# Optimization experiments

Measured on AMD Instinct MI355X. Metric: run time of the kernel, lower is better.

The kernel has to match this reference:

```python
import jax, jax.numpy as jnp
import numpy as np

EPS = 1e-5

def _lin(x, w, b):
    return x @ w + b

def _ln(x, scale, bias):
    m = jnp.mean(x, axis=-1, keepdims=True)
    v = jnp.var(x, axis=-1, keepdims=True)
    return (x - m) / jnp.sqrt(v + EPS) * scale + bias

def setup_inputs() -> dict:
    key = jax.random.key(0)
    B, N, F, OUT, TRI = 4, 128, 128, 128, 8
    ks = iter(jax.random.split(key, 64))
    def lin_params(fan_in, fan_out):
        s = 1.0 / np.sqrt(fan_in)
        w = jax.random.uniform(next(ks), (fan_in, fan_out), minval=-s, maxval=s, dtype=jnp.float32)
        b = jax.random.uniform(next(ks), (fan_out,), minval=-s, maxval=s, dtype=jnp.float32)
        return w, b
    inp = {}
    inp['node_fts'] = jax.random.normal(next(ks), (B, N, F), dtype=jnp.float32)
    inp['edge_fts'] = jax.random.normal(next(ks), (B, N, N, F), dtype=jnp.float32)
    inp['graph_fts'] = jax.random.normal(next(ks), (B, F), dtype=jnp.float32)
    inp['hidden'] = jax.random.normal(next(ks), (B, N, F), dtype=jnp.float32)
    inp['adj_matrix'] = jax.random.randint(next(ks), (B, N, N), 0, 2, dtype=jnp.int32)
    inp['m1_w'], inp['m1_b'] = lin_params(2 * F, OUT)
    inp['m2_w'], inp['m2_b'] = lin_params(2 * F, OUT)
    inp['me_w'], inp['me_b'] = lin_params(F, OUT)
    inp['mg_w'], inp['mg_b'] = lin_params(F, OUT)
    inp['mlp1_w'], inp['mlp1_b'] = lin_params(OUT, OUT)
    inp['mlp2_w'], inp['mlp2_b'] = lin_params(OUT, OUT)
    inp['o1_w'], inp['o1_b'] = lin_params(2 * F, OUT)
    inp['o2_w'], inp['o2_b'] = lin_params(OUT, OUT)
    inp['t1_w'], inp['t1_b'] = lin_params(2 * F, TRI)
    inp['t2_w'], inp['t2_b'] = lin_params(2 * F, TRI)
    inp['te1_w'], inp['te1_b'] = lin_params(F, TRI)
    inp['te2_w'], inp['te2_b'] = lin_params(F, TRI)
    inp['te3_w'], inp['te3_b'] = lin_params(F, TRI)
    inp['tg_w'], inp['tg_b'] = lin_params(F, TRI)
    inp['o3_w'], inp['o3_b'] = lin_params(TRI, OUT)
    inp['norm_scale'] = jnp.ones((OUT,), dtype=jnp.float32)
    inp['norm_bias'] = jnp.zeros((OUT,), dtype=jnp.float32)
    return inp

def reference(node_fts, edge_fts, graph_fts, hidden, adj_matrix,
              m1_w, m1_b, m2_w, m2_b, me_w, me_b, mg_w, mg_b,
              mlp1_w, mlp1_b, mlp2_w, mlp2_b,
              o1_w, o1_b, o2_w, o2_b,
              t1_w, t1_b, t2_w, t2_b,
              te1_w, te1_b, te2_w, te2_b, te3_w, te3_b,
              tg_w, tg_b, o3_w, o3_b, norm_scale, norm_bias):
    z = jnp.concatenate([node_fts, hidden], axis=-1)          # [B,N,2F]
    msg_1 = _lin(z, m1_w, m1_b)                                # [B,N,H]
    msg_2 = _lin(z, m2_w, m2_b)
    msg_e = _lin(edge_fts, me_w, me_b)                         # [B,N,N,H]
    msg_g = _lin(graph_fts, mg_w, mg_b)                        # [B,H]
    msgs = msg_1[:, None, :, :] + msg_2[:, :, None, :] + msg_e + msg_g[:, None, None, :]
    # msg_mlp: ReLU -> Linear -> ReLU -> Linear
    msgs = _lin(jax.nn.relu(_lin(jax.nn.relu(msgs), mlp1_w, mlp1_b)), mlp2_w, mlp2_b)
    # triplet messages (note: original code reuses t_1 for tri_3 -- faithful)
    tri_1 = _lin(z, t1_w, t1_b)                                # [B,N,T]
    tri_2 = _lin(z, t2_w, t2_b)
    tri_3 = _lin(z, t1_w, t1_b)
    tri_e_1 = _lin(edge_fts, te1_w, te1_b)                     # [B,N,N,T]
    tri_e_2 = _lin(edge_fts, te2_w, te2_b)
    tri_e_3 = _lin(edge_fts, te3_w, te3_b)
    tri_g = _lin(graph_fts, tg_w, tg_b)                        # [B,T]
    triplets = (tri_1[:, :, None, None, :] + tri_2[:, None, :, None, :]
                + tri_3[:, None, None, :, :]
                + tri_e_1[:, :, :, None, :] + tri_e_2[:, :, None, :, :]
                + tri_e_3[:, None, :, :, :]
                + tri_g[:, None, None, None, :])               # [B,N,N,N,T]
    tri_msgs = _lin(jnp.max(triplets, axis=1), o3_w, o3_b)     # [B,N,N,OUT]
    tri_msgs = _ln(jax.nn.relu(tri_msgs), norm_scale, norm_bias)
    # masked max aggregation
    maxarg = jnp.where(adj_matrix[..., None] == 1, msgs, -1e9)
    msgs_agg = jnp.max(maxarg, axis=1)                         # [B,N,H]
    out = jax.nn.relu(_lin(z, o1_w, o1_b) + _lin(msgs_agg, o2_w, o2_b))
    out = _ln(out, norm_scale, norm_bias)
    return out, tri_msgs
```

## Files before the change

kernel.cpp:

```cpp
#include <hip/hip_runtime.h>
#include <hip/hip_bf16.h>
#include <cstddef>
#include <cstdint>
#include <cstring>

typedef __attribute__((ext_vector_type(8))) short bf16x8;
typedef __attribute__((ext_vector_type(4))) float f32x4;
typedef unsigned short ushort_t;

__device__ __forceinline__ ushort_t f2b(float f) {
    uint32_t x = __float_as_uint(f);
    uint32_t r = (x + 0x7FFFu + ((x >> 16) & 1u)) >> 16;
    return (ushort_t)r;
}
__device__ __forceinline__ float b2f(ushort_t u) {
    return __uint_as_float(((uint32_t)u) << 16);
}
__device__ __forceinline__ uint32_t pk2(float x, float y) {
    __hip_bfloat162 h = __float22bfloat162_rn(float2{x, y});
    uint32_t u;
    __builtin_memcpy(&u, &h, 4);
    return u;
}

__global__ void prep_kernel(const float* __restrict__ m1_w, const float* __restrict__ m2_w,
                            const float* __restrict__ o1_w, const float* __restrict__ t1_w,
                            const float* __restrict__ t2_w,
                            const float* __restrict__ me_w, const float* __restrict__ mlp1_w,
                            const float* __restrict__ mlp2_w,
                            const float* __restrict__ te1_w, const float* __restrict__ te2_w,
                            const float* __restrict__ te3_w,
                            const float* __restrict__ graph_fts,
                            const float* __restrict__ mg_w, const float* __restrict__ mg_b,
                            const float* __restrict__ m1_b,
                            const float* __restrict__ tg_w, const float* __restrict__ t2_b,
                            const float* __restrict__ tg_b,
                            ushort_t* __restrict__ Wnt,
                            ushort_t* __restrict__ Wme, ushort_t* __restrict__ Wm1,
                            ushort_t* __restrict__ Wm2, ushort_t* __restrict__ TEt,
                            float* __restrict__ G1, float* __restrict__ TG) {
    int idx = blockIdx.x * 256 + threadIdx.x;
    if (idx < 106496) {
        int o = idx >> 8, k = idx & 255;
        float v = 0.0f;
        if (o < 128)       v = m1_w[k * 128 + o];
        else if (o < 256)  v = m2_w[k * 128 + (o - 128)];
        else if (o < 384)  v = o1_w[k * 128 + (o - 256)];
        else if (o < 392)  v = t1_w[k * 8 + (o - 384)];
        else if (o < 400)  v = t2_w[k * 8 + (o - 392)];
        Wnt[idx] = f2b(v);
    } else if (idx < 122880) {
        int t = idx - 106496, o = t >> 7, h = t & 127;
        Wme[t] = f2b(me_w[h * 128 + o]);
    } else if (idx < 139264) {
        int t = idx - 122880, o = t >> 7, h = t & 127;
        Wm1[t] = f2b(mlp1_w[h * 128 + o]);
    } else if (idx < 155648) {
        int t = idx - 139264, o = t >> 7, h = t & 127;
        Wm2[t] = f2b(mlp2_w[h * 128 + o]);
    } else if (idx < 159744) {
        int t = idx - 155648, c = t >> 7, h = t & 127;
        float v = 0.0f;
        if (c < 8)       v = te1_w[h * 8 + c];
        else if (c < 16) v = te2_w[h * 8 + (c - 8)];
        else if (c < 24) v = te3_w[h * 8 + (c - 16)];
        TEt[t] = f2b(v);
    } else if (idx < 160256) {
        int t = idx - 159744, b = t >> 7, h = t & 127;
        float a = m1_b[h] + mg_b[h];
        #pragma unroll 4
        for (int k = 0; k < 128; k++) a = fmaf(graph_fts[b * 128 + k], mg_w[k * 128 + h], a);
        G1[t] = a;
    } else if (idx < 160288) {
        int t = idx - 160256, b = t >> 3, tt = t & 7;
        float a = t2_b[tt] + tg_b[tt];
        #pragma unroll 4
        for (int k = 0; k < 128; k++) a = fmaf(graph_fts[b * 128 + k], tg_w[k * 8 + tt], a);
        TG[t] = a;
    }
}

__global__ __launch_bounds__(256)
void node_gemm(const float* __restrict__ node_fts, const float* __restrict__ hidden,
               const ushort_t* __restrict__ Wnt,
               const float* __restrict__ G1, const float* __restrict__ m2_b,
               const float* __restrict__ o1_b, const float* __restrict__ t1_b,
               const float* __restrict__ TG,
               float* __restrict__ M1, float* __restrict__ M2, float* __restrict__ O1z,
               float* __restrict__ T1v, float* __restrict__ TT2) {
    __shared__ ushort_t Zs[32 * 256];
    char* Zb = (char*)Zs;
    const int tid = threadIdx.x;
    const int blk = blockIdx.x;
    const int rowblk = blk >> 1, colh = blk & 1;
    const int b = rowblk >> 2, q = rowblk & 3;
    const int row0 = b * 128 + q * 32;
    const int w = tid >> 6, l = tid & 63, g = l >> 4, lq = l & 15;

    const float4* nsrc = reinterpret_cast<const float4*>(node_fts + (size_t)row0 * 128);
    const float4* hsrc = reinterpret_cast<const float4*>(hidden + (size_t)row0 * 128);
    #pragma unroll
    for (int p = 0; p < 8; p++) {
        int idx = tid + p * 256;
        int r = idx >> 6, c4 = idx & 63;
        float4 v = (c4 < 32) ? nsrc[r * 32 + c4] : hsrc[r * 32 + (c4 - 32)];
        uint2 pk;
        pk.x = pk2(v.x, v.y);
        pk.y = pk2(v.z, v.w);
        *reinterpret_cast<uint2*>(Zb + r * 512 + (((c4 >> 1) ^ (r & 7)) << 4) + (c4 & 1) * 8) = pk;
    }
    __syncthreads();

    for (int mt = colh * 13 + w; mt < colh * 13 + 13; mt += 4) {
        f32x4 acc0 = (f32x4){0.f, 0.f, 0.f, 0.f};
        f32x4 acc1 = (f32x4){0.f, 0.f, 0.f, 0.f};
        const ushort_t* arow = Wnt + (size_t)(mt * 16 + lq) * 256;
        #pragma unroll
        for (int ks = 0; ks < 8; ks++) {
            bf16x8 a = *reinterpret_cast<const bf16x8*>(arow + ks * 32 + g * 8);
            int j0 = lq, j1 = 16 + lq;
            bf16x8 b0 = *reinterpret_cast<const bf16x8*>(Zb + j0 * 512 + (((ks * 4 + g) ^ (j0 & 7)) << 4));
            bf16x8 b1 = *reinterpret_cast<const bf16x8*>(Zb + j1 * 512 + (((ks * 4 + g) ^ (j1 & 7)) << 4));
            acc0 = __builtin_amdgcn_mfma_f32_16x16x32_bf16(a, b0, acc0, 0, 0, 0);
            acc1 = __builtin_amdgcn_mfma_f32_16x16x32_bf16(a, b1, acc1, 0, 0, 0);
        }
        #pragma unroll
        for (int half = 0; half < 2; half++) {
            const f32x4 acc = half ? acc1 : acc0;
            const int grow = row0 + half * 16 + lq;
            #pragma unroll
            for (int c = 0; c < 4; c++) {
                int o = mt * 16 + g * 4 + c;
                float v = acc[c];
                if (o < 128)       M1[(size_t)grow * 128 + o] = v + G1[b * 128 + o];
                else if (o < 256)  M2[(size_t)grow * 128 + (o - 128)] = v + m2_b[o - 128];
                else if (o < 384)  O1z[(size_t)grow * 128 + (o - 256)] = v + o1_b[o - 256];
                else if (o < 392)  T1v[(size_t)grow * 8 + (o - 384)] = v + t1_b[o - 384];
                else if (o < 400)  TT2[(size_t)grow * 8 + (o - 392)] = v + TG[b * 8 + (o - 392)];
            }
        }
    }
}

__device__ __forceinline__ void mmv(const ushort_t* __restrict__ Wt, const char* Xa,
                                    f32x4 acc[2][4], int o_blk, int j_blk, int g, int lq) {
    #pragma unroll
    for (int ks = 0; ks < 4; ks++) {
        bf16x8 a[2], bb[4];
        #pragma unroll
        for (int m = 0; m < 2; m++)
            a[m] = *reinterpret_cast<const bf16x8*>(Wt + (size_t)(o_blk + m * 16 + lq) * 128 + ks * 32 + g * 8);
        #pragma unroll
        for (int n = 0; n < 4; n++) {
            int j = j_blk + n * 16 + lq;
            bb[n] = *reinterpret_cast<const bf16x8*>(Xa + j * 256 + (((ks * 4 + g) ^ (j & 7)) << 4));
        }
        #pragma unroll
        for (int m = 0; m < 2; m++)
            #pragma unroll
            for (int n = 0; n < 4; n++)
                acc[m][n] = __builtin_amdgcn_mfma_f32_16x16x32_bf16(a[m], bb[n], acc[m][n], 0, 0, 0);
    }
}

__global__ __launch_bounds__(512, 4)
void edge_kernel(const float* __restrict__ edge_fts,
                 const ushort_t* __restrict__ Wme, const float* __restrict__ me_b,
                 const ushort_t* __restrict__ Wm1, const float* __restrict__ mlp1_b,
                 const ushort_t* __restrict__ Wm2, const float* __restrict__ mlp2_b,
                 const ushort_t* __restrict__ TEt,
                 const float* __restrict__ te1_b, const float* __restrict__ te2_b,
                 const float* __restrict__ te3_b,
                 const float* __restrict__ M1,  const float* __restrict__ M2,
                 const float* __restrict__ T1v, const float* __restrict__ TT2,
                 const int* __restrict__ adj, const float* __restrict__ O1z,
                 const float* __restrict__ o2_w, const float* __restrict__ o2_b,
                 const float* __restrict__ nsc, const float* __restrict__ nbi,
                 float* __restrict__ out,
                 ushort_t* __restrict__ T1buf, ushort_t* __restrict__ T2buf,
                 ushort_t* __restrict__ E3buf) {
    __shared__ ushort_t Xs[2][16384];
    char* X0 = (char*)Xs[0];
    char* X1 = (char*)Xs[1];
    const int tid = threadIdx.x;
    const int b  = blockIdx.x >> 7;
    const int jf = blockIdx.x & 127;
    const int w = tid >> 6, l = tid & 63, g = l >> 4, lq = l & 15;
    const int o_blk = (w & 3) * 32, j_blk = (w >> 2) * 64;

    #pragma unroll
    for (int p = 0; p < 8; p++) {
        int idx = tid + p * 512;
        int r = idx >> 5, c4 = idx & 31;
        const float4* src = reinterpret_cast<const float4*>(
            edge_fts + ((size_t)(b * 128 + r) * 128 + jf) * 128);
        float4 v = src[c4];
        uint2 pk;
        pk.x = pk2(v.x, v.y);
        pk.y = pk2(v.z, v.w);
        *reinterpret_cast<uint2*>(X0 + r * 256 + (((c4 >> 1) ^ (r & 7)) << 4) + (c4 & 1) * 8) = pk;
    }
    __syncthreads();

    {
        const int m_te = w & 1;
        const int jq = (w >> 1) & 3;
        const ushort_t* At = TEt + m_te * 16 * 128;
        f32x4 acc2[2];
        #pragma unroll
        for (int n = 0; n < 2; n++) acc2[n] = (f32x4){0.f, 0.f, 0.f, 0.f};
        #pragma unroll
        for (int ks = 0; ks < 4; ks++) {
            bf16x8 a = *reinterpret_cast<const bf16x8*>(At + lq * 128 + ks * 32 + g * 8);
            #pragma unroll
            for (int n = 0; n < 2; n++) {
                int j = jq * 32 + n * 16 + lq;
                bf16x8 bbv = *reinterpret_cast<const bf16x8*>(X0 + j * 256 + (((ks * 4 + g) ^ (j & 7)) << 4));
                acc2[n] = __builtin_amdgcn_mfma_f32_16x16x32_bf16(a, bbv, acc2[n], 0, 0, 0);
            }
        }
        if (m_te == 0) {
            if (g < 2) {
                int t0 = g * 4;
                const float4 eb = *reinterpret_cast<const float4*>(te1_b + t0);
                #pragma unroll
                for (int n = 0; n < 2; n++) {
                    int r = jq * 32 + n * 16 + lq;
                    const float4 tv = *reinterpret_cast<const float4*>(T1v + (size_t)(b * 128 + r) * 8 + t0);
                    uint2 pkv;
                    pkv.x = pk2(acc2[n][0] + eb.x + tv.x, acc2[n][1] + eb.y + tv.y);
                    pkv.y = pk2(acc2[n][2] + eb.z + tv.z, acc2[n][3] + eb.w + tv.w);
                    *reinterpret_cast<uint2*>(T1buf + ((size_t)(b * 128 + jf) * 128 + r) * 8 + t0) = pkv;
                }
            } else {
                int t0 = g * 4 - 8;
                const float4 eb = *reinterpret_cast<const float4*>(te2_b + t0);
                #pragma unroll
                for (int n = 0; n < 2; n++) {
                    int r = jq * 32 + n * 16 + lq;
                    uint2 pkv;
                    pkv.x = pk2(acc2[n][0] + eb.x, acc2[n][1] + eb.y);
                    pkv.y = pk2(acc2[n][2] + eb.z, acc2[n][3] + eb.w);
                    *reinterpret_cast<uint2*>(T2buf + ((size_t)(b * 128 + r) * 128 + jf) * 8 + t0) = pkv;
                }
            }
        } else if (g < 2) {
            int t0 = g * 4;
            const float4 eb = *reinterpret_cast<const float4*>(te3_b + t0);
            const float4 t3v = *reinterpret_cast<const float4*>(T1v + (size_t)(b * 128 + jf) * 8 + t0);
            #pragma unroll
            for (int n = 0; n < 2; n++) {
                int r = jq * 32 + n * 16 + lq;
                const float4 t2v = *reinterpret_cast<const float4*>(TT2 + (size_t)(b * 128 + r) * 8 + t0);
                uint2 pkv;
                pkv.x = pk2(acc2[n][0] + eb.x + t2v.x + t3v.x, acc2[n][1] + eb.y + t2v.y + t3v.y);
                pkv.y = pk2(acc2[n][2] + eb.z + t2v.z + t3v.z, acc2[n][3] + eb.w + t2v.w + t3v.w);
                *reinterpret_cast<uint2*>(E3buf + ((size_t)(b * 128 + r) * 128 + jf) * 8 + t0) = pkv;
            }
        }
    }

    f32x4 acc[2][4];

    #pragma unroll
    for (int m = 0; m < 2; m++)
        #pragma unroll
        for (int n = 0; n < 4; n++) acc[m][n] = (f32x4){0.f, 0.f, 0.f, 0.f};
    mmv(Wme, X0, acc, o_blk, j_blk, g, lq);
    {
        #pragma unroll
        for (int m = 0; m < 2; m++) {
            int o0 = o_blk + m * 16 + g * 4;
            const float4 eb = *reinterpret_cast<const float4*>(me_b + o0);
            const float4 m1 = *reinterpret_cast<const float4*>(M1 + (size_t)(b * 128 + jf) * 128 + o0);
            float4 bc = make_float4(eb.x + m1.x, eb.y + m1.y, eb.z + m1.z, eb.w + m1.w);
            #pragma unroll
            for (int n = 0; n < 4; n++) {
                int j = j_blk + n * 16 + lq;
                const float4 m2 = *reinterpret_cast<const float4*>(M2 + (size_t)(b * 128 + j) * 128 + o0);
                float r0 = fmaxf(acc[m][n][0] + bc.x + m2.x, 0.f);
                float r1 = fmaxf(acc[m][n][1] + bc.y + m2.y, 0.f);
                float r2 = fmaxf(acc[m][n][2] + bc.z + m2.z, 0.f);
                float r3 = fmaxf(acc[m][n][3] + bc.w + m2.w, 0.f);
                uint2 pk;
                pk.x = pk2(r0, r1);
                pk.y = pk2(r2, r3);
                *reinterpret_cast<uint2*>(X1 + j * 256 + ((((o0 >> 3) ^ (j & 7))) << 4) + (o0 & 7) * 2) = pk;
            }
        }
        __syncthreads();
    }

    #pragma unroll
    for (int m = 0; m < 2; m++)
        #pragma unroll
        for (int n = 0; n < 4; n++) acc[m][n] = (f32x4){0.f, 0.f, 0.f, 0.f};
    mmv(Wm1, X1, acc, o_blk, j_blk, g, lq);
    {
        #pragma unroll
        for (int m = 0; m < 2; m++) {
            int o0 = o_blk + m * 16 + g * 4;
            const float4 bb = *reinterpret_cast<const float4*>(mlp1_b + o0);
            #pragma unroll
            for (int n = 0; n < 4; n++) {
                int j = j_blk + n * 16 + lq;
                float r0 = fmaxf(acc[m][n][0] + bb.x, 0.f);
                float r1 = fmaxf(acc[m][n][1] + bb.y, 0.f);
                float r2 = fmaxf(acc[m][n][2] + bb.z, 0.f);
                float r3 = fmaxf(acc[m][n][3] + bb.w, 0.f);
                uint2 pk;
                pk.x = pk2(r0, r1);
                pk.y = pk2(r2, r3);
                *reinterpret_cast<uint2*>(X0 + j * 256 + ((((o0 >> 3) ^ (j & 7))) << 4) + (o0 & 7) * 2) = pk;
            }
        }
        __syncthreads();
    }

    #pragma unroll
    for (int m = 0; m < 2; m++)
        #pragma unroll
        for (int n = 0; n < 4; n++) acc[m][n] = (f32x4){0.f, 0.f, 0.f, 0.f};
    mmv(Wm2, X0, acc, o_blk, j_blk, g, lq);
    {
        #pragma unroll
        for (int m = 0; m < 2; m++) {
            int o0 = o_blk + m * 16 + g * 4;
            const float4 bb = *reinterpret_cast<const float4*>(mlp2_b + o0);
            #pragma unroll
            for (int n = 0; n < 4; n++) {
                int j = j_blk + n * 16 + lq;
                float r0 = acc[m][n][0] + bb.x;
                float r1 = acc[m][n][1] + bb.y;
                float r2 = acc[m][n][2] + bb.z;
                float r3 = acc[m][n][3] + bb.w;
                uint2 pk;
                pk.x = pk2(r0, r1);
                pk.y = pk2(r2, r3);
                *reinterpret_cast<uint2*>(X1 + j * 256 + ((((o0 >> 3) ^ (j & 7))) << 4) + (o0 & 7) * 2) = pk;
            }
        }
        __syncthreads();
    }

    {
        float* scr  = reinterpret_cast<float*>(X0);
        float* aggs = scr;
        float* fagg = scr + 512;
        float* sums = scr + 640;
        const int h = tid & 127, wv = tid >> 7;
        float o1zv0 = 0.f, o1zv1 = 0.f, ob0 = 0.f, ob1 = 0.f;
        float sc0 = 0.f, sc1 = 0.f, bi0 = 0.f, bi1 = 0.f;
        if (w == 0) {
            const float* o1p = O1z + (size_t)(b * 128 + jf) * 128;
            o1zv0 = o1p[l];      o1zv1 = o1p[l + 64];
            ob0 = o2_b[l];       ob1 = o2_b[l + 64];
            sc0 = nsc[l];        sc1 = nsc[l + 64];
            bi0 = nbi[l];        bi1 = nbi[l + 64];
        }
        {
            const int* acol = adj + b * 16384 + jf;
            float amax = -1e9f;
            #pragma unroll 8
            for (int s = 0; s < 32; s++) {
                int r = wv * 32 + s;
                ushort_t u = *reinterpret_cast<const ushort_t*>(
                    X1 + r * 256 + (((h >> 3) ^ (r & 7)) << 4) + (h & 7) * 2);
                amax = (acol[r * 128] == 1) ? fmaxf(amax, b2f(u)) : amax;
            }
            aggs[wv * 128 + h] = amax;
        }
        __syncthreads();
        if (tid < 128)
            fagg[tid] = fmaxf(fmaxf(aggs[tid], aggs[128 + tid]),
                              fmaxf(aggs[256 + tid], aggs[384 + tid]));
        __syncthreads();
        {
            float part = 0.f;
            const float* wcol = o2_w + h;
            #pragma unroll 8
            for (int k = wv * 32; k < wv * 32 + 32; k++)
                part = fmaf(fagg[k], wcol[k * 128], part);
            sums[wv * 128 + h] = part;
        }
        __syncthreads();
        if (w == 0) {
            float v0 = fmaxf(ob0 + o1zv0 + sums[l] + sums[128 + l] + sums[256 + l] + sums[384 + l], 0.f);
            float v1 = fmaxf(ob1 + o1zv1 + sums[l + 64] + sums[128 + l + 64] + sums[256 + l + 64] + sums[384 + l + 64], 0.f);
            float s = v0 + v1, s2 = v0 * v0 + v1 * v1;
            #pragma unroll
            for (int off = 32; off >= 1; off >>= 1) {
                s  += __shfl_xor(s, off, 64);
                s2 += __shfl_xor(s2, off, 64);
            }
            const float mean = s * (1.0f / 128.0f);
            const float var = s2 * (1.0f / 128.0f) - mean * mean;
            const float rstd = rsqrtf(var + 1e-5f);
            float* dst = out + (size_t)(b * 128 + jf) * 128;
            dst[l]      = (v0 - mean) * rstd * sc0 + bi0;
            dst[l + 64] = (v1 - mean) * rstd * sc1 + bi1;
        }
    }
}

__global__ __launch_bounds__(512)
void tri_kernel(const ushort_t* __restrict__ T1buf, const ushort_t* __restrict__ T2buf,
                const ushort_t* __restrict__ E3buf, const float* __restrict__ o3_w,
                const float* __restrict__ o3_b, const float* __restrict__ scale,
                const float* __restrict__ bias, float* __restrict__ tri_out) {
    __shared__ __align__(16) float T1s[1024];
    __shared__ __align__(16) float E3s[1024];
    __shared__ __align__(16) float o3s[1024];
    __shared__ __align__(16) float Ps[4][128][8];
    const int b = blockIdx.x >> 7, jf = blockIdx.x & 127;
    const int tid = threadIdx.x;
    if (tid < 128) {
        uint4 u = reinterpret_cast<const uint4*>(T1buf + (size_t)(b * 128 + jf) * 1024)[tid];
        float* d = &T1s[tid * 8];
        d[0] = b2f((ushort_t)u.x); d[1] = b2f((ushort_t)(u.x >> 16));
        d[2] = b2f((ushort_t)u.y); d[3] = b2f((ushort_t)(u.y >> 16));
        d[4] = b2f((ushort_t)u.z); d[5] = b2f((ushort_t)(u.z >> 16));
        d[6] = b2f((ushort_t)u.w); d[7] = b2f((ushort_t)(u.w >> 16));
    } else if (tid < 256) {
        int t = tid - 128;
        uint4 u = reinterpret_cast<const uint4*>(E3buf + (size_t)(b * 128 + jf) * 1024)[t];
        float* d = &E3s[t * 8];
        d[0] = b2f((ushort_t)u.x); d[1] = b2f((ushort_t)(u.x >> 16));
        d[2] = b2f((ushort_t)u.y); d[3] = b2f((ushort_t)(u.y >> 16));
        d[4] = b2f((ushort_t)u.z); d[5] = b2f((ushort_t)(u.z >> 16));
        d[6] = b2f((ushort_t)u.w); d[7] = b2f((ushort_t)(u.w >> 16));
    } else {
        int t = tid - 256;
        reinterpret_cast<float4*>(o3s)[t] = reinterpret_cast<const float4*>(o3_w)[t];
    }
    __syncthreads();

    {
        const int kf = tid & 127, ih = tid >> 7;
        float a8[8];
        #pragma unroll
        for (int t = 0; t < 8; t++) a8[t] = -3.0e38f;
        const uint4* t2p = reinterpret_cast<const uint4*>(T2buf + (size_t)b * 131072);
        #pragma unroll 4
        for (int ii = 0; ii < 32; ++ii) {
            const int i = ih * 32 + ii;
            uint4 u = t2p[i * 128 + kf];
            const float* t1r = &T1s[i * 8];
            a8[0] = fmaxf(a8[0], t1r[0] + b2f((ushort_t)u.x));
            a8[1] = fmaxf(a8[1], t1r[1] + b2f((ushort_t)(u.x >> 16)));
            a8[2] = fmaxf(a8[2], t1r[2] + b2f((ushort_t)u.y));
            a8[3] = fmaxf(a8[3], t1r[3] + b2f((ushort_t)(u.y >> 16)));
            a8[4] = fmaxf(a8[4], t1r[4] + b2f((ushort_t)u.z));
            a8[5] = fmaxf(a8[5], t1r[5] + b2f((ushort_t)(u.z >> 16)));
            a8[6] = fmaxf(a8[6], t1r[6] + b2f((ushort_t)u.w));
            a8[7] = fmaxf(a8[7], t1r[7] + b2f((ushort_t)(u.w >> 16)));
        }
        #pragma unroll
        for (int t = 0; t < 8; t++) Ps[ih][kf][t] = a8[t];
    }
    __syncthreads();

    const int w = tid >> 6, l = tid & 63;
    const float ob0 = o3_b[l],     ob1 = o3_b[l + 64];
    const float sc0 = scale[l],    sc1 = scale[l + 64];
    const float bi0 = bias[l],     bi1 = bias[l + 64];
    for (int kk = 0; kk < 16; ++kk) {
        const int kf = w * 16 + kk;
        float m8[8];
        #pragma unroll
        for (int t = 0; t < 8; t++)
            m8[t] = fmaxf(fmaxf(Ps[0][kf][t], Ps[1][kf][t]),
                          fmaxf(Ps[2][kf][t], Ps[3][kf][t])) + E3s[kf * 8 + t];
        float v0 = ob0, v1 = ob1;
        #pragma unroll
        for (int t = 0; t < 8; t++) {
            v0 = fmaf(m8[t], o3s[t * 128 + l], v0);
            v1 = fmaf(m8[t], o3s[t * 128 + l + 64], v1);
        }
        v0 = fmaxf(v0, 0.0f);
        v1 = fmaxf(v1, 0.0f);
        float s = v0 + v1, s2 = v0 * v0 + v1 * v1;
        #pragma unroll
        for (int off = 32; off >= 1; off >>= 1) {
            s  += __shfl_xor(s, off, 64);
            s2 += __shfl_xor(s2, off, 64);
        }
        const float mean = s * (1.0f / 128.0f);
        const float var = s2 * (1.0f / 128.0f) - mean * mean;
        const float rstd = rsqrtf(var + 1e-5f);
        float* dst = tri_out + (size_t)((b * 128 + jf) * 128 + kf) * 128;
        dst[l]      = (v0 - mean) * rstd * sc0 + bi0;
        dst[l + 64] = (v1 - mean) * rstd * sc1 + bi1;
    }
}

extern "C" void kernel_launch(void* const* d_in, const int* in_sizes, int n_in,
                              void* d_out, int out_size, void* d_ws, size_t ws_size,
                              hipStream_t stream) {
    const float* node_fts  = (const float*)d_in[0];
    const float* edge_fts  = (const float*)d_in[1];
    const float* graph_fts = (const float*)d_in[2];
    const float* hidden    = (const float*)d_in[3];
    const int*   adj       = (const int*)d_in[4];
    const float* m1_w = (const float*)d_in[5],  *m1_b = (const float*)d_in[6];
    const float* m2_w = (const float*)d_in[7],  *m2_b = (const float*)d_in[8];
    const float* me_w = (const float*)d_in[9],  *me_b = (const float*)d_in[10];
    const float* mg_w = (const float*)d_in[11], *mg_b = (const float*)d_in[12];
    const float* mlp1_w = (const float*)d_in[13], *mlp1_b = (const float*)d_in[14];
    const float* mlp2_w = (const float*)d_in[15], *mlp2_b = (const float*)d_in[16];
    const float* o1_w = (const float*)d_in[17], *o1_b = (const float*)d_in[18];
    const float* o2_w = (const float*)d_in[19], *o2_b = (const float*)d_in[20];
    const float* t1_w = (const float*)d_in[21], *t1_b = (const float*)d_in[22];
    const float* t2_w = (const float*)d_in[23], *t2_b = (const float*)d_in[24];
    const float* te1_w = (const float*)d_in[25], *te1_b = (const float*)d_in[26];
    const float* te2_w = (const float*)d_in[27], *te2_b = (const float*)d_in[28];
    const float* te3_w = (const float*)d_in[29], *te3_b = (const float*)d_in[30];
    const float* tg_w = (const float*)d_in[31], *tg_b = (const float*)d_in[32];
    const float* o3_w = (const float*)d_in[33], *o3_b = (const float*)d_in[34];
    const float* norm_scale = (const float*)d_in[35];
    const float* norm_bias  = (const float*)d_in[36];

    char* w8 = (char*)d_ws;
    float*    M1    = (float*)(w8 + 0);
    float*    M2    = (float*)(w8 + 262144);
    float*    O1z   = (float*)(w8 + 524288);
    float*    T1v   = (float*)(w8 + 786432);
    float*    TT2   = (float*)(w8 + 802816);
    ushort_t* Wme   = (ushort_t*)(w8 + 819200);
    ushort_t* Wm1   = (ushort_t*)(w8 + 851968);
    ushort_t* Wm2   = (ushort_t*)(w8 + 884736);
    ushort_t* TEt   = (ushort_t*)(w8 + 917504);
    ushort_t* T1buf = (ushort_t*)(w8 + 17702912);
    ushort_t* T2buf = (ushort_t*)(w8 + 19800064);
    ushort_t* E3buf = (ushort_t*)(w8 + 21897216);
    ushort_t* Wnt   = (ushort_t*)(w8 + 23994368);
    float*    G1    = (float*)(w8 + 24207360);
    float*    TG    = (float*)(w8 + 24209408);

    float* out_p  = (float*)d_out;
    float* tri_p  = (float*)d_out + 65536;

    prep_kernel<<<627, 256, 0, stream>>>(m1_w, m2_w, o1_w, t1_w, t2_w,
                                         me_w, mlp1_w, mlp2_w, te1_w, te2_w, te3_w,
                                         graph_fts, mg_w, mg_b, m1_b, tg_w, t2_b, tg_b,
                                         Wnt, Wme, Wm1, Wm2, TEt, G1, TG);
    node_gemm<<<32, 256, 0, stream>>>(node_fts, hidden, Wnt, G1, m2_b, o1_b, t1_b, TG,
                                      M1, M2, O1z, T1v, TT2);
    edge_kernel<<<512, 512, 0, stream>>>(edge_fts, Wme, me_b, Wm1, mlp1_b, Wm2, mlp2_b,
                                         TEt, te1_b, te2_b, te3_b,
                                         M1, M2, T1v, TT2,
                                         adj, O1z, o2_w, o2_b, norm_scale, norm_bias,
                                         out_p, T1buf, T2buf, E3buf);
    tri_kernel<<<512, 512, 0, stream>>>(T1buf, T2buf, E3buf, o3_w, o3_b,
                                        norm_scale, norm_bias, tri_p);
}
```

Before: 89.76 us.

## Give each wave a private 16-row strip to drop block barriers in edge MLP chain

Each wave now owns 16 edge rows and computes all 128 outputs for them, so the edge tile, the me/mlp1/mlp2 chain, and the triplet-edge projections read only wave-local LDS data. This removes the intermediate __syncthreads, halves the LDS footprint with a single in-place buffer plus a small scratch array, and keeps the B operand in registers across all output tiles. The cost is that every wave reloads the full weight matrices from global/L1 (8 A-fragment loads per k-step instead of 2), and accumulator register use grows.

```diff
diff --git a/kernel.cpp b/kernel.cpp
--- a/kernel.cpp
+++ b/kernel.cpp
@@ -142,24 +142,17 @@
     }
 }
 
-__device__ __forceinline__ void mmv(const ushort_t* __restrict__ Wt, const char* Xa,
-                                    f32x4 acc[2][4], int o_blk, int j_blk, int g, int lq) {
+__device__ __forceinline__ void mm_strip(const ushort_t* __restrict__ Wt,
+                                         const bf16x8 breg[4], f32x4 acc[8],
+                                         int g, int lq) {
     #pragma unroll
     for (int ks = 0; ks < 4; ks++) {
-        bf16x8 a[2], bb[4];
-        #pragma unroll
-        for (int m = 0; m < 2; m++)
-            a[m] = *reinterpret_cast<const bf16x8*>(Wt + (size_t)(o_blk + m * 16 + lq) * 128 + ks * 32 + g * 8);
-        #pragma unroll
-        for (int n = 0; n < 4; n++) {
-            int j = j_blk + n * 16 + lq;
-            bb[n] = *reinterpret_cast<const bf16x8*>(Xa + j * 256 + (((ks * 4 + g) ^ (j & 7)) << 4));
-        }
-        #pragma unroll
-        for (int m = 0; m < 2; m++)
-            #pragma unroll
-            for (int n = 0; n < 4; n++)
-                acc[m][n] = __builtin_amdgcn_mfma_f32_16x16x32_bf16(a[m], bb[n], acc[m][n], 0, 0, 0);
+        #pragma unroll
+        for (int m = 0; m < 8; m++) {
+            bf16x8 a = *reinterpret_cast<const bf16x8*>(
+                Wt + (size_t)(m * 16 + lq) * 128 + ks * 32 + g * 8);
+            acc[m] = __builtin_amdgcn_mfma_f32_16x16x32_bf16(a, breg[ks], acc[m], 0, 0, 0);
+        }
     }
 }
 
@@ -179,172 +172,147 @@
                  float* __restrict__ out,
                  ushort_t* __restrict__ T1buf, ushort_t* __restrict__ T2buf,
                  ushort_t* __restrict__ E3buf) {
-    __shared__ ushort_t Xs[2][16384];
-    char* X0 = (char*)Xs[0];
-    char* X1 = (char*)Xs[1];
+    __shared__ ushort_t Xs[16384];
+    __shared__ float scr[1152];
+    char* X = (char*)Xs;
     const int tid = threadIdx.x;
     const int b  = blockIdx.x >> 7;
     const int jf = blockIdx.x & 127;
     const int w = tid >> 6, l = tid & 63, g = l >> 4, lq = l & 15;
-    const int o_blk = (w & 3) * 32, j_blk = (w >> 2) * 64;
+    const int strip = w * 16;
+    const int jrow = strip + lq;
 
     #pragma unroll
     for (int p = 0; p < 8; p++) {
-        int idx = tid + p * 512;
-        int r = idx >> 5, c4 = idx & 31;
+        int fidx = l + p * 64;
+        int r = strip + (fidx >> 5), c4 = fidx & 31;
         const float4* src = reinterpret_cast<const float4*>(
             edge_fts + ((size_t)(b * 128 + r) * 128 + jf) * 128);
         float4 v = src[c4];
         uint2 pk;
         pk.x = pk2(v.x, v.y);
         pk.y = pk2(v.z, v.w);
-        *reinterpret_cast<uint2*>(X0 + r * 256 + (((c4 >> 1) ^ (r & 7)) << 4) + (c4 & 1) * 8) = pk;
+        *reinterpret_cast<uint2*>(X + r * 256 + (((c4 >> 1) ^ (r & 7)) << 4) + (c4 & 1) * 8) = pk;
+    }
+
+    bf16x8 breg[4];
+    #pragma unroll
+    for (int ks = 0; ks < 4; ks++)
+        breg[ks] = *reinterpret_cast<const bf16x8*>(
+            X + jrow * 256 + (((ks * 4 + g) ^ (jrow & 7)) << 4));
+
+    {
+        f32x4 acc2[2];
+        acc2[0] = (f32x4){0.f, 0.f, 0.f, 0.f};
+        acc2[1] = (f32x4){0.f, 0.f, 0.f, 0.f};
+        #pragma unroll
+        for (int ks = 0; ks < 4; ks++) {
+            #pragma unroll
+            for (int m2 = 0; m2 < 2; m2++) {
+                bf16x8 a = *reinterpret_cast<const bf16x8*>(
+                    TEt + (size_t)(m2 * 16 + lq) * 128 + ks * 32 + g * 8);
+                acc2[m2] = __builtin_amdgcn_mfma_f32_16x16x32_bf16(a, breg[ks], acc2[m2], 0, 0, 0);
+            }
+        }
+        const int r = jrow;
+        if (g < 2) {
+            int t0 = g * 4;
+            const float4 eb = *reinterpret_cast<const float4*>(te1_b + t0);
+            const float4 tv = *reinterpret_cast<const float4*>(T1v + (size_t)(b * 128 + r) * 8 + t0);
+            uint2 pkv;
+            pkv.x = pk2(acc2[0][0] + eb.x + tv.x, acc2[0][1] + eb.y + tv.y);
+            pkv.y = pk2(acc2[0][2] + eb.z + tv.z, acc2[0][3] + eb.w + tv.w);
+            *reinterpret_cast<uint2*>(T1buf + ((size_t)(b * 128 + jf) * 128 + r) * 8 + t0) = pkv;
+            const float4 eb3 = *reinterpret_cast<const float4*>(te3_b + t0);
+            const float4 t3v = *reinterpret_cast<const float4*>(T1v + (size_t)(b * 128 + jf) * 8 + t0);
+            const float4 t2v = *reinterpret_cast<const float4*>(TT2 + (size_t)(b * 128 + r) * 8 + t0);
+            uint2 pk3;
+            pk3.x = pk2(acc2[1][0] + eb3.x + t2v.x + t3v.x, acc2[1][1] + eb3.y + t2v.y + t3v.y);
+            pk3.y = pk2(acc2[1][2] + eb3.z + t2v.z + t3v.z, acc2[1][3] + eb3.w + t2v.w + t3v.w);
+            *reinterpret_cast<uint2*>(E3buf + ((size_t)(b * 128 + r) * 128 + jf) * 8 + t0) = pk3;
+        } else {
+            int t0 = g * 4 - 8;
+            const float4 eb = *reinterpret_cast<const float4*>(te2_b + t0);
+            uint2 pkv;
+            pkv.x = pk2(acc2[0][0] + eb.x, acc2[0][1] + eb.y);
+            pkv.y = pk2(acc2[0][2] + eb.z, acc2[0][3] + eb.w);
+            *reinterpret_cast<uint2*>(T2buf + ((size_t)(b * 128 + r) * 128 + jf) * 8 + t0) = pkv;
+        }
+    }
+
+    f32x4 acc[8];
+
+    #pragma unroll
+    for (int m = 0; m < 8; m++) acc[m] = (f32x4){0.f, 0.f, 0.f, 0.f};
+    mm_strip(Wme, breg, acc, g, lq);
+    {
+        const float* m1p = M1 + (size_t)(b * 128 + jf) * 128;
+        const float* m2p = M2 + (size_t)(b * 128 + jrow) * 128;
+        #pragma unroll
+        for (int m = 0; m < 8; m++) {
+            int o0 = m * 16 + g * 4;
+            const float4 eb = *reinterpret_cast<const float4*>(me_b + o0);
+            const float4 m1v = *reinterpret_cast<const float4*>(m1p + o0);
+            const float4 m2v = *reinterpret_cast<const float4*>(m2p + o0);
+            float r0 = fmaxf(acc[m][0] + eb.x + m1v.x + m2v.x, 0.f);
+            float r1 = fmaxf(acc[m][1] + eb.y + m1v.y + m2v.y, 0.f);
+            float r2 = fmaxf(acc[m][2] + eb.z + m1v.z + m2v.z, 0.f);
+            float r3 = fmaxf(acc[m][3] + eb.w + m1v.w + m2v.w, 0.f);
+            uint2 pk;
+            pk.x = pk2(r0, r1);
+            pk.y = pk2(r2, r3);
+            *reinterpret_cast<uint2*>(X + jrow * 256 + ((((o0 >> 3) ^ (jrow & 7))) << 4) + (o0 & 7) * 2) = pk;
+        }
+    }
+    #pragma unroll
+    for (int ks = 0; ks < 4; ks++)
+        breg[ks] = *reinterpret_cast<const bf16x8*>(
+            X + jrow * 256 + (((ks * 4 + g) ^ (jrow & 7)) << 4));
+
+    #pragma unroll
+    for (int m = 0; m < 8; m++) acc[m] = (f32x4){0.f, 0.f, 0.f, 0.f};
+    mm_strip(Wm1, breg, acc, g, lq);
+    {
+        #pragma unroll
+        for (int m = 0; m < 8; m++) {
+            int o0 = m * 16 + g * 4;
+            const float4 bb = *reinterpret_cast<const float4*>(mlp1_b + o0);
+            float r0 = fmaxf(acc[m][0] + bb.x, 0.f);
+            float r1 = fmaxf(acc[m][1] + bb.y, 0.f);
+            float r2 = fmaxf(acc[m][2] + bb.z, 0.f);
+            float r3 = fmaxf(acc[m][3] + bb.w, 0.f);
+            uint2 pk;
+            pk.x = pk2(r0, r1);
+            pk.y = pk2(r2, r3);
+            *reinterpret_cast<uint2*>(X + jrow * 256 + ((((o0 >> 3) ^ (jrow & 7))) << 4) + (o0 & 7) * 2) = pk;
+        }
+    }
+    #pragma unroll
+    for (int ks = 0; ks < 4; ks++)
+        breg[ks] = *reinterpret_cast<const bf16x8*>(
+            X + jrow * 256 + (((ks * 4 + g) ^ (jrow & 7)) << 4));
+
+    #pragma unroll
+    for (int m = 0; m < 8; m++) acc[m] = (f32x4){0.f, 0.f, 0.f, 0.f};
+    mm_strip(Wm2, breg, acc, g, lq);
+    {
+        #pragma unroll
+        for (int m = 0; m < 8; m++) {
+            int o0 = m * 16 + g * 4;
+            const float4 bb = *reinterpret_cast<const float4*>(mlp2_b + o0);
+            float r0 = acc[m][0] + bb.x;
+            float r1 = acc[m][1] + bb.y;
+            float r2 = acc[m][2] + bb.z;
+            float r3 = acc[m][3] + bb.w;
+            uint2 pk;
+            pk.x = pk2(r0, r1);
+            pk.y = pk2(r2, r3);
+            *reinterpret_cast<uint2*>(X + jrow * 256 + ((((o0 >> 3) ^ (jrow & 7))) << 4) + (o0 & 7) * 2) = pk;
+        }
     }
     __syncthreads();
 
     {
-        const int m_te = w & 1;
-        const int jq = (w >> 1) & 3;
-        const ushort_t* At = TEt + m_te * 16 * 128;
-        f32x4 acc2[2];
-        #pragma unroll
-        for (int n = 0; n < 2; n++) acc2[n] = (f32x4){0.f, 0.f, 0.f, 0.f};
-        #pragma unroll
-        for (int ks = 0; ks < 4; ks++) {
-            bf16x8 a = *reinterpret_cast<const bf16x8*>(At + lq * 128 + ks * 32 + g * 8);
-            #pragma unroll
-            for (int n = 0; n < 2; n++) {
-                int j = jq * 32 + n * 16 + lq;
-                bf16x8 bbv = *reinterpret_cast<const bf16x8*>(X0 + j * 256 + (((ks * 4 + g) ^ (j & 7)) << 4));
-                acc2[n] = __builtin_amdgcn_mfma_f32_16x16x32_bf16(a, bbv, acc2[n], 0, 0, 0);
-            }
-        }
-        if (m_te == 0) {
-            if (g < 2) {
-                int t0 = g * 4;
-                const float4 eb = *reinterpret_cast<const float4*>(te1_b + t0);
-                #pragma unroll
-                for (int n = 0; n < 2; n++) {
-                    int r = jq * 32 + n * 16 + lq;
-                    const float4 tv = *reinterpret_cast<const float4*>(T1v + (size_t)(b * 128 + r) * 8 + t0);
-                    uint2 pkv;
-                    pkv.x = pk2(acc2[n][0] + eb.x + tv.x, acc2[n][1] + eb.y + tv.y);
-                    pkv.y = pk2(acc2[n][2] + eb.z + tv.z, acc2[n][3] + eb.w + tv.w);
-                    *reinterpret_cast<uint2*>(T1buf + ((size_t)(b * 128 + jf) * 128 + r) * 8 + t0) = pkv;
-                }
-            } else {
-                int t0 = g * 4 - 8;
-                const float4 eb = *reinterpret_cast<const float4*>(te2_b + t0);
-                #pragma unroll
-                for (int n = 0; n < 2; n++) {
-                    int r = jq * 32 + n * 16 + lq;
-                    uint2 pkv;
-                    pkv.x = pk2(acc2[n][0] + eb.x, acc2[n][1] + eb.y);
-                    pkv.y = pk2(acc2[n][2] + eb.z, acc2[n][3] + eb.w);
-                    *reinterpret_cast<uint2*>(T2buf + ((size_t)(b * 128 + r) * 128 + jf) * 8 + t0) = pkv;
-                }
-            }
-        } else if (g < 2) {
-            int t0 = g * 4;
-            const float4 eb = *reinterpret_cast<const float4*>(te3_b + t0);
-            const float4 t3v = *reinterpret_cast<const float4*>(T1v + (size_t)(b * 128 + jf) * 8 + t0);
-            #pragma unroll
-            for (int n = 0; n < 2; n++) {
-                int r = jq * 32 + n * 16 + lq;
-                const float4 t2v = *reinterpret_cast<const float4*>(TT2 + (size_t)(b * 128 + r) * 8 + t0);
-                uint2 pkv;
-                pkv.x = pk2(acc2[n][0] + eb.x + t2v.x + t3v.x, acc2[n][1] + eb.y + t2v.y + t3v.y);
-                pkv.y = pk2(acc2[n][2] + eb.z + t2v.z + t3v.z, acc2[n][3] + eb.w + t2v.w + t3v.w);
-                *reinterpret_cast<uint2*>(E3buf + ((size_t)(b * 128 + r) * 128 + jf) * 8 + t0) = pkv;
-            }
-        }
-    }
-
-    f32x4 acc[2][4];
-
-    #pragma unroll
-    for (int m = 0; m < 2; m++)
-        #pragma unroll
-        for (int n = 0; n < 4; n++) acc[m][n] = (f32x4){0.f, 0.f, 0.f, 0.f};
-    mmv(Wme, X0, acc, o_blk, j_blk, g, lq);
-    {
-        #pragma unroll
-        for (int m = 0; m < 2; m++) {
-            int o0 = o_blk + m * 16 + g * 4;
-            const float4 eb = *reinterpret_cast<const float4*>(me_b + o0);
-            const float4 m1 = *reinterpret_cast<const float4*>(M1 + (size_t)(b * 128 + jf) * 128 + o0);
-            float4 bc = make_float4(eb.x + m1.x, eb.y + m1.y, eb.z + m1.z, eb.w + m1.w);
-            #pragma unroll
-            for (int n = 0; n < 4; n++) {
-                int j = j_blk + n * 16 + lq;
-                const float4 m2 = *reinterpret_cast<const float4*>(M2 + (size_t)(b * 128 + j) * 128 + o0);
-                float r0 = fmaxf(acc[m][n][0] + bc.x + m2.x, 0.f);
-                float r1 = fmaxf(acc[m][n][1] + bc.y + m2.y, 0.f);
-                float r2 = fmaxf(acc[m][n][2] + bc.z + m2.z, 0.f);
-                float r3 = fmaxf(acc[m][n][3] + bc.w + m2.w, 0.f);
-                uint2 pk;
-                pk.x = pk2(r0, r1);
-                pk.y = pk2(r2, r3);
-                *reinterpret_cast<uint2*>(X1 + j * 256 + ((((o0 >> 3) ^ (j & 7))) << 4) + (o0 & 7) * 2) = pk;
-            }
-        }
-        __syncthreads();
-    }
-
-    #pragma unroll
-    for (int m = 0; m < 2; m++)
-        #pragma unroll
-        for (int n = 0; n < 4; n++) acc[m][n] = (f32x4){0.f, 0.f, 0.f, 0.f};
-    mmv(Wm1, X1, acc, o_blk, j_blk, g, lq);
-    {
-        #pragma unroll
-        for (int m = 0; m < 2; m++) {
-            int o0 = o_blk + m * 16 + g * 4;
-            const float4 bb = *reinterpret_cast<const float4*>(mlp1_b + o0);
-            #pragma unroll
-            for (int n = 0; n < 4; n++) {
-                int j = j_blk + n * 16 + lq;
-                float r0 = fmaxf(acc[m][n][0] + bb.x, 0.f);
-                float r1 = fmaxf(acc[m][n][1] + bb.y, 0.f);
-                float r2 = fmaxf(acc[m][n][2] + bb.z, 0.f);
-                float r3 = fmaxf(acc[m][n][3] + bb.w, 0.f);
-                uint2 pk;
-                pk.x = pk2(r0, r1);
-                pk.y = pk2(r2, r3);
-                *reinterpret_cast<uint2*>(X0 + j * 256 + ((((o0 >> 3) ^ (j & 7))) << 4) + (o0 & 7) * 2) = pk;
-            }
-        }
-        __syncthreads();
-    }
-
-    #pragma unroll
-    for (int m = 0; m < 2; m++)
-        #pragma unroll
-        for (int n = 0; n < 4; n++) acc[m][n] = (f32x4){0.f, 0.f, 0.f, 0.f};
-    mmv(Wm2, X0, acc, o_blk, j_blk, g, lq);
-    {
-        #pragma unroll
-        for (int m = 0; m < 2; m++) {
-            int o0 = o_blk + m * 16 + g * 4;
-            const float4 bb = *reinterpret_cast<const float4*>(mlp2_b + o0);
-            #pragma unroll
-            for (int n = 0; n < 4; n++) {
-                int j = j_blk + n * 16 + lq;
-                float r0 = acc[m][n][0] + bb.x;
-                float r1 = acc[m][n][1] + bb.y;
-                float r2 = acc[m][n][2] + bb.z;
-                float r3 = acc[m][n][3] + bb.w;
-                uint2 pk;
-                pk.x = pk2(r0, r1);
-                pk.y = pk2(r2, r3);
-                *reinterpret_cast<uint2*>(X1 + j * 256 + ((((o0 >> 3) ^ (j & 7))) << 4) + (o0 & 7) * 2) = pk;
-            }
-        }
-        __syncthreads();
-    }
-
-    {
-        float* scr  = reinterpret_cast<float*>(X0);
         float* aggs = scr;
         float* fagg = scr + 512;
         float* sums = scr + 640;
@@ -365,7 +333,7 @@
             for (int s = 0; s < 32; s++) {
                 int r = wv * 32 + s;
                 ushort_t u = *reinterpret_cast<const ushort_t*>(
-                    X1 + r * 256 + (((h >> 3) ^ (r & 7)) << 4) + (h & 7) * 2);
+                    X + r * 256 + (((h >> 3) ^ (r & 7)) << 4) + (h & 7) * 2);
                 amax = (acol[r * 128] == 1) ? fmaxf(amax, b2f(u)) : amax;
             }
             aggs[wv * 128 + h] = amax;
```

Result: slower. 125.5 us (+39.8%).
